# Kernel tuning notes

Hardware: AMD Instinct MI355X
Metric: run time of the kernel (lower is better)

The kernel has to match this reference:

```python
import jax, jax.numpy as jnp
import numpy as np

N, D_IN, D_C, D_Q, K = 4096, 64, 32, 128, 3


def setup_inputs() -> dict:
    key = jax.random.key(0)
    ks = jax.random.split(key, 16)
    rn = lambda k, shp, s: jax.random.normal(k, shp, dtype=jnp.float32) * s
    inp = {
        "x": rn(ks[0], (N, D_IN), 1.0),
        "comms": rn(ks[1], (N, D_C), 0.1),
        # dense positive transition matrix (all entries nonzero -> the
        # trans==0 -> -inf masking step is a faithful no-op here)
        "trans": jax.random.uniform(ks[2], (N, N), dtype=jnp.float32, minval=0.01, maxval=1.0),
        "mask": jnp.ones((N,), dtype=jnp.int32),
        # encoding: Linear(num_inputs + comm_channels, ch_q)
        "W_enc": rn(ks[3], (D_IN + D_C, D_Q), 1.0 / np.sqrt(D_IN + D_C)),
        "b_enc": rn(ks[4], (D_Q,), 0.01),
        # att_decoding[k]: Linear(ch_q, ch_q)
        "W_ad": rn(ks[5], (K, D_Q, D_Q), 1.0 / np.sqrt(D_Q)),
        "b_ad": rn(ks[6], (K, D_Q), 0.01),
        # att[k]: Linear(2*ch_q, 1)
        "w_att": rn(ks[7], (K, 2 * D_Q), 1.0 / np.sqrt(2 * D_Q)),
        "b_att": rn(ks[8], (K,), 0.01),
        # att_vectors[k]: Linear(ch_q, ch_q)
        "W_av": rn(ks[9], (K, D_Q, D_Q), 1.0 / np.sqrt(D_Q)),
        "b_av": rn(ks[10], (K, D_Q), 0.01),
        # decoding: Linear(ch_q, 1)
        "W_dec": rn(ks[11], (D_Q,), 1.0 / np.sqrt(D_Q)),
        "b_dec": rn(ks[12], (), 0.01),
    }
    return inp


def reference(x, comms, trans, mask, W_enc, b_enc, W_ad, b_ad, w_att, b_att,
              W_av, b_av, W_dec, b_dec):
    dq = W_ad.shape[-1]
    # encoding of [node features, communication vector]
    h = jnp.concatenate([x, comms], axis=-1) @ W_enc + b_enc          # (n, dq)
    # trans.transpose(0,1); zeros -> -inf (additive log-mask)
    tb = trans.T
    tb = jnp.where(tb == 0, -jnp.inf, tb)                              # (n, n)
    for k in range(K):
        att = h @ W_ad[k] + b_ad[k]                                    # (n, dq)
        # concat-GAT score: score[i,j] = w_a . att[j] + w_b . att[i] + b
        # (decomposition of Linear(cat(att_t, att_t^T)) -> avoids n x n x 2dq)
        wa, wb = w_att[k, :dq], w_att[k, dq:]
        score = (att @ wb)[:, None] + (att @ wa)[None, :] + b_att[k]   # (n, n)
        focus = jax.nn.softmax(score + tb, axis=1)                     # (n, n)
        v = h @ W_av[k] + b_av[k]                                      # (n, dq)
        h = focus @ v                                                  # (n, dq)
    out = h @ W_dec + b_dec                                            # (n,)
    # final masking (args.rl = False branch): masked nodes -> -inf
    s = out + jnp.where(mask == 0, -jnp.inf, 0.0).astype(out.dtype)
    return s
```

## Files before the change

kernel.cpp:

```cpp
#include <hip/hip_runtime.h>
#include <math.h>

#define N 4096
#define DQ 128
#define DIN 64
#define DC 32
#define NT 9
#define PST9 144
#define PST1 16
#define NIT 256
#define KB 4
#define SW 8
#define ELS 260

typedef __attribute__((ext_vector_type(8))) short short8;
typedef __attribute__((ext_vector_type(8))) _Float16 half8;
typedef __attribute__((ext_vector_type(4))) float f32x4;

__device__ __forceinline__ unsigned short f2h(float x) {
  return __builtin_bit_cast(unsigned short, (_Float16)x);
}
__device__ __forceinline__ void async16(unsigned short* lds, const unsigned short* g) {
  __builtin_amdgcn_global_load_lds(
      (const __attribute__((address_space(1))) void*)g,
      (__attribute__((address_space(3))) void*)lds, 16, 0, 0);
}

__global__ __launch_bounds__(256) void kExp(const float* __restrict__ trans,
                                            unsigned short* __restrict__ Ef) {
  __shared__ float sh[32 * ELS];
  const int tid = threadIdx.x;
  const int ip = blockIdx.x;
  const int kt = blockIdx.y;
  float4 v[8];
#pragma unroll
  for (int p = 0; p < 8; ++p) {
    const int f = p * 256 + tid;
    const int r = f >> 6, c = (f & 63) << 2;
    v[p] = *(const float4*)&trans[((size_t)kt * 32 + r) * N + ip * 256 + c];
  }
#pragma unroll
  for (int p = 0; p < 8; ++p) {
    const int f = p * 256 + tid;
    const int r = f >> 6, c = (f & 63) << 2;
    float4 e;
    e.x = __expf(v[p].x); e.y = __expf(v[p].y);
    e.z = __expf(v[p].z); e.w = __expf(v[p].w);
    *(float4*)&sh[r * ELS + c] = e;
  }
  __syncthreads();
  const int w = tid >> 6, lane = tid & 63;
  const int quad = lane >> 4, l15 = lane & 15;
#pragma unroll
  for (int s = 0; s < 4; ++s) {
    const int col = 64 * w + s * 16 + l15;
    unsigned short hb[8];
#pragma unroll
    for (int jj = 0; jj < 8; ++jj)
      hb[jj] = f2h(sh[(quad * 8 + jj) * ELS + col]);
    const short8 sv = {(short)hb[0], (short)hb[1], (short)hb[2], (short)hb[3],
                       (short)hb[4], (short)hb[5], (short)hb[6], (short)hb[7]};
    const int it = ip * 16 + 4 * w + s;
    *(short8*)(Ef + (((size_t)kt * NIT + it) * 64 + lane) * 8) = sv;
  }
}

__device__ __forceinline__ void v_phase(const float* hs_row, float p,
    const float* __restrict__ W_av_k, const float* __restrict__ b_av_k,
    int r, int d4, unsigned short* shh) {
  float a[4] = {b_av_k[d4], b_av_k[d4 + 1], b_av_k[d4 + 2], b_av_k[d4 + 3]};
  for (int c = 0; c < DQ; ++c) {
    const float hv = hs_row[c];
    const float4 w = *(const float4*)&W_av_k[c * DQ + d4];
    a[0] += hv * w.x; a[1] += hv * w.y; a[2] += hv * w.z; a[3] += hv * w.w;
  }
  const int nt = d4 >> 4;
#pragma unroll
  for (int e = 0; e < 4; ++e)
    shh[nt * 128 + ((d4 + e) & 15) * 8 + r] = f2h(p * a[e]);
  const int c32 = d4 >> 2;
  if (c32 < 16)
    shh[8 * 128 + c32 * 8 + r] = (c32 == 0) ? f2h(p) : 0;
}

__device__ __forceinline__ void v_store(int tid, int blk,
    const unsigned short* shh, unsigned short* __restrict__ Vf) {
  const int kt = blk >> 2, quad = blk & 3;
  if (tid < NT * 16) {
    const int nt = tid >> 4, l15 = tid & 15;
    const size_t dst = (((size_t)kt * NT + nt) * 64 + quad * 16 + l15) * 8;
    *(short8*)(Vf + dst) = *(const short8*)&shh[nt * 128 + l15 * 8];
  }
}

__global__ __launch_bounds__(256) void kVS0(const float* __restrict__ x,
    const float* __restrict__ comms, const float* __restrict__ W_enc,
    const float* __restrict__ b_enc, const float* __restrict__ W_ad_k,
    const float* __restrict__ wa, const float* __restrict__ W_av_k,
    const float* __restrict__ b_av_k, unsigned short* __restrict__ Vf) {
  __shared__ float xs[8][96];
  __shared__ float hs[8][DQ];
  __shared__ float u[DQ];
  __shared__ float pb[8];
  __shared__ __align__(16) unsigned short shh[NT * 128];
  const int tid = threadIdx.x;
  const int blk = blockIdx.x;
  if (tid < 128) {
    const float4 v = *(const float4*)&x[(size_t)blk * 8 * DIN + tid * 4];
    const int idx = tid * 4, r = idx >> 6, c = idx & 63;
    xs[r][c] = v.x; xs[r][c + 1] = v.y; xs[r][c + 2] = v.z; xs[r][c + 3] = v.w;
  } else if (tid < 192) {
    const int t = tid - 128;
    const float4 v = *(const float4*)&comms[(size_t)blk * 8 * DC + t * 4];
    const int idx = t * 4, r = idx >> 5, c = idx & 31;
    xs[r][64 + c] = v.x; xs[r][64 + c + 1] = v.y; xs[r][64 + c + 2] = v.z; xs[r][64 + c + 3] = v.w;
  }
  if (tid < DQ) {
    float s = 0.f;
    const float* wrow = &W_ad_k[tid * DQ];
    for (int q = 0; q < DQ; ++q) s += wrow[q] * wa[q];
    u[tid] = s;
  }
  __syncthreads();
  const int r = tid >> 5;
  const int c32 = tid & 31;
  const int d4 = c32 * 4;
  {
    float a0 = b_enc[d4], a1 = b_enc[d4 + 1], a2 = b_enc[d4 + 2], a3 = b_enc[d4 + 3];
    for (int c = 0; c < 96; ++c) {
      const float hv = xs[r][c];
      const float4 w = *(const float4*)&W_enc[c * DQ + d4];
      a0 += hv * w.x; a1 += hv * w.y; a2 += hv * w.z; a3 += hv * w.w;
    }
    hs[r][d4] = a0; hs[r][d4 + 1] = a1; hs[r][d4 + 2] = a2; hs[r][d4 + 3] = a3;
  }
  __syncthreads();
  float part = 0.f;
  for (int c = c32; c < DQ; c += 32) part += hs[r][c] * u[c];
#pragma unroll
  for (int m = 16; m > 0; m >>= 1) part += __shfl_xor(part, m, 32);
  if (c32 == 0) pb[r] = __expf(part);
  __syncthreads();
  v_phase(hs[r], pb[r], W_av_k, b_av_k, r, d4, shh);
  __syncthreads();
  v_store(tid, blk, shh, Vf);
}

__global__ __launch_bounds__(256) void kVSR(const float* __restrict__ P,
    const float* __restrict__ W_ad_k, const float* __restrict__ wa,
    const float* __restrict__ W_av_k, const float* __restrict__ b_av_k,
    unsigned short* __restrict__ Vf) {
  __shared__ float hs[8][DQ];
  __shared__ float u[DQ];
  __shared__ float pb[8];
  __shared__ __align__(16) unsigned short shh[NT * 128];
  const int tid = threadIdx.x;
  const int r = tid >> 5;
  const int c32 = tid & 31;
  const int d4 = c32 * 4;
  const int j = blockIdx.x * 8 + r;
  if (tid < DQ) {
    float s = 0.f;
    const float* wrow = &W_ad_k[tid * DQ];
    for (int q = 0; q < DQ; ++q) s += wrow[q] * wa[q];
    u[tid] = s;
  }
  float4 num = {0.f, 0.f, 0.f, 0.f};
  float den = 0.f;
#pragma unroll
  for (int s = 0; s < KB; ++s) {
    const float* b = &P[((size_t)s * N + j) * PST9];
    const float4 v = *(const float4*)&b[d4];
    num.x += v.x; num.y += v.y; num.z += v.z; num.w += v.w;
    den += b[128];
  }
  const float inv = 1.f / den;
  hs[r][d4] = num.x * inv; hs[r][d4 + 1] = num.y * inv;
  hs[r][d4 + 2] = num.z * inv; hs[r][d4 + 3] = num.w * inv;
  __syncthreads();
  float part = 0.f;
  for (int c = c32; c < DQ; c += 32) part += hs[r][c] * u[c];
#pragma unroll
  for (int m = 16; m > 0; m >>= 1) part += __shfl_xor(part, m, 32);
  if (c32 == 0) pb[r] = __expf(part);
  __syncthreads();
  v_phase(hs[r], pb[r], W_av_k, b_av_k, r, d4, shh);
  __syncthreads();
  v_store(tid, blockIdx.x, shh, Vf);
}

__global__ __launch_bounds__(256) void kVSRc(const float* __restrict__ P,
    const float* __restrict__ W_ad_k, const float* __restrict__ wa,
    const float* __restrict__ W_av_k, const float* __restrict__ b_av_k,
    const float* __restrict__ W_dec, unsigned short* __restrict__ Vc) {
  __shared__ float hs[8][DQ];
  __shared__ float u[DQ];
  __shared__ float pb[8];
  const int tid = threadIdx.x;
  const int r = tid >> 5;
  const int c32 = tid & 31;
  const int d4 = c32 * 4;
  const int j = blockIdx.x * 8 + r;
  if (tid < DQ) {
    float s = 0.f;
    const float* wrow = &W_ad_k[tid * DQ];
    for (int q = 0; q < DQ; ++q) s += wrow[q] * wa[q];
    u[tid] = s;
  }
  float4 num = {0.f, 0.f, 0.f, 0.f};
  float den = 0.f;
#pragma unroll
  for (int s = 0; s < KB; ++s) {
    const float* b = &P[((size_t)s * N + j) * PST9];
    const float4 v = *(const float4*)&b[d4];
    num.x += v.x; num.y += v.y; num.z += v.z; num.w += v.w;
    den += b[128];
  }
  const float inv = 1.f / den;
  hs[r][d4] = num.x * inv; hs[r][d4 + 1] = num.y * inv;
  hs[r][d4 + 2] = num.z * inv; hs[r][d4 + 3] = num.w * inv;
  __syncthreads();
  float part = 0.f;
  for (int c = c32; c < DQ; c += 32) part += hs[r][c] * u[c];
#pragma unroll
  for (int m = 16; m > 0; m >>= 1) part += __shfl_xor(part, m, 32);
  if (c32 == 0) pb[r] = __expf(part);
  __syncthreads();
  float a[4] = {b_av_k[d4], b_av_k[d4 + 1], b_av_k[d4 + 2], b_av_k[d4 + 3]};
  for (int c = 0; c < DQ; ++c) {
    const float hv = hs[r][c];
    const float4 w = *(const float4*)&W_av_k[c * DQ + d4];
    a[0] += hv * w.x; a[1] += hv * w.y; a[2] += hv * w.z; a[3] += hv * w.w;
  }
  float vd = a[0] * W_dec[d4] + a[1] * W_dec[d4 + 1]
           + a[2] * W_dec[d4 + 2] + a[3] * W_dec[d4 + 3];
#pragma unroll
  for (int m = 16; m > 0; m >>= 1) vd += __shfl_xor(vd, m, 32);
  const float p = pb[r];
  if (c32 < 16) {
    const int blk = blockIdx.x;
    const size_t ix = (((size_t)(blk >> 2)) * 64 + (blk & 3) * 16 + c32) * 8 + r;
    Vc[ix] = (c32 == 0) ? f2h(p * vd) : (c32 == 1) ? f2h(p) : 0;
  }
}

template <int NTT, int PST>
__global__ __launch_bounds__(256) void kGemmR(
    const unsigned short* __restrict__ Ef, const unsigned short* __restrict__ Vf,
    float* __restrict__ P) {
  __shared__ __align__(16) unsigned short lds[4 * 2 * NTT * 512];
  const int tid = threadIdx.x;
  const int w = tid >> 6, lane = tid & 63;
  const int quad = lane >> 4, l15 = lane & 15;
  const int it0 = blockIdx.x * 2;
  const size_t ktw = (size_t)blockIdx.y * (4 * SW) + w * SW;
  unsigned short* myL = lds + w * (2 * NTT * 512);

  f32x4 acc[2][NTT];
#pragma unroll
  for (int ti = 0; ti < 2; ++ti)
#pragma unroll
    for (int nt = 0; nt < NTT; ++nt) acc[ti][nt] = (f32x4){0.f, 0.f, 0.f, 0.f};

#pragma unroll
  for (int c = 0; c < NTT; ++c)
    async16(myL + c * 512, Vf + (ktw * NTT + c) * 512 + lane * 8);
  half8 A0[2], A1[2];
#pragma unroll
  for (int ti = 0; ti < 2; ++ti)
    A0[ti] = __builtin_bit_cast(half8,
        *(const short8*)(Ef + ((ktw * NIT + it0 + ti) * 64 + lane) * 8));

#pragma unroll
  for (int t = 0; t < SW; ++t) {
    if (t + 1 < SW) {
      const size_t ktn = ktw + t + 1;
#pragma unroll
      for (int c = 0; c < NTT; ++c)
        async16(myL + ((t + 1) & 1) * NTT * 512 + c * 512,
                Vf + (ktn * NTT + c) * 512 + lane * 8);
#pragma unroll
      for (int ti = 0; ti < 2; ++ti)
        A1[ti] = __builtin_bit_cast(half8,
            *(const short8*)(Ef + ((ktn * NIT + it0 + ti) * 64 + lane) * 8));
      __builtin_amdgcn_s_waitcnt(0xF70 | (NTT + 2));
    } else {
      __builtin_amdgcn_s_waitcnt(0xF70);
    }
    const unsigned short* bb = myL + (t & 1) * NTT * 512;
#pragma unroll
    for (int nt = 0; nt < NTT; ++nt) {
      const half8 Bh = __builtin_bit_cast(half8,
          *(const short8*)(bb + nt * 512 + lane * 8));
      acc[0][nt] = __builtin_amdgcn_mfma_f32_16x16x32_f16(A0[0], Bh, acc[0][nt], 0, 0, 0);
      acc[1][nt] = __builtin_amdgcn_mfma_f32_16x16x32_f16(A0[1], Bh, acc[1][nt], 0, 0, 0);
    }
    if (t + 1 < SW) { A0[0] = A1[0]; A0[1] = A1[1]; }
  }
  __syncthreads();
  float* lf = (float*)lds;
#pragma unroll
  for (int ti = 0; ti < 2; ++ti)
#pragma unroll
    for (int nt = 0; nt < NTT; ++nt) {
      float4 v; v.x = acc[ti][nt][0]; v.y = acc[ti][nt][1];
      v.z = acc[ti][nt][2]; v.w = acc[ti][nt][3];
      *(float4*)&lf[(w * 2 * NTT + ti * NTT + nt) * 256 + lane * 4] = v;
    }
  __syncthreads();
  float* Pb = P + (size_t)blockIdx.y * N * PST;
  for (int p = w; p < 2 * NTT; p += 4) {
    const int ti = p / NTT, nt = p % NTT;
    float4 s = {0.f, 0.f, 0.f, 0.f};
#pragma unroll
    for (int wv = 0; wv < 4; ++wv) {
      const float4 v = *(const float4*)&lf[(wv * 2 * NTT + p) * 256 + lane * 4];
      s.x += v.x; s.y += v.y; s.z += v.z; s.w += v.w;
    }
    const float sr[4] = {s.x, s.y, s.z, s.w};
    if (NTT == 1 || nt != 8 || l15 == 0) {
#pragma unroll
      for (int r = 0; r < 4; ++r) {
        const int i = (it0 + ti) * 16 + quad * 4 + r;
        Pb[(size_t)i * PST + nt * 16 + l15] = sr[r];
      }
    }
  }
}

__global__ __launch_bounds__(256) void kOut(const float* __restrict__ P3,
    const float* __restrict__ b_dec, const int* __restrict__ mask,
    float* __restrict__ out) {
  const int i = blockIdx.x * 256 + threadIdx.x;
  float num = 0.f, den = 0.f;
#pragma unroll
  for (int s = 0; s < KB; ++s) {
    const float* b = &P3[((size_t)s * N + i) * PST1];
    num += b[0];
    den += b[1];
  }
  out[i] = (mask[i] == 0) ? -INFINITY : num / den + b_dec[0];
}

extern "C" void kernel_launch(void* const* d_in, const int* in_sizes, int n_in,
                              void* d_out, int out_size, void* d_ws, size_t ws_size,
                              hipStream_t stream) {
  (void)in_sizes; (void)n_in; (void)out_size; (void)ws_size;
  const float* x     = (const float*)d_in[0];
  const float* comms = (const float*)d_in[1];
  const float* trans = (const float*)d_in[2];
  const int*   mask  = (const int*)d_in[3];
  const float* W_enc = (const float*)d_in[4];
  const float* b_enc = (const float*)d_in[5];
  const float* W_ad  = (const float*)d_in[6];
  const float* w_att = (const float*)d_in[8];
  const float* W_av  = (const float*)d_in[10];
  const float* b_av  = (const float*)d_in[11];
  const float* W_dec = (const float*)d_in[12];
  const float* b_dec = (const float*)d_in[13];
  float* out         = (float*)d_out;

  char* ws = (char*)d_ws;
  unsigned short* Vf = (unsigned short*)ws;  ws += (size_t)(N / 32) * NT * 512 * 2;
  unsigned short* Vc = (unsigned short*)ws;  ws += (size_t)(N / 32) * 512 * 2;
  unsigned short* Ef = (unsigned short*)ws;  ws += (size_t)N * N * 2;
  float* P  = (float*)ws;                    ws += (size_t)KB * N * PST9 * 4;
  float* P3 = (float*)ws;

  kExp<<<dim3(16, 128), 256, 0, stream>>>(trans, Ef);
  kVS0<<<N / 8, 256, 0, stream>>>(x, comms, W_enc, b_enc, W_ad, w_att,
                                  W_av, b_av, Vf);
  kGemmR<NT, PST9><<<dim3(NIT / 2, KB), 256, 0, stream>>>(Ef, Vf, P);

  kVSR<<<N / 8, 256, 0, stream>>>(P, W_ad + (size_t)1 * DQ * DQ,
                                  w_att + 2 * DQ, W_av + (size_t)1 * DQ * DQ,
                                  b_av + DQ, Vf);
  kGemmR<NT, PST9><<<dim3(NIT / 2, KB), 256, 0, stream>>>(Ef, Vf, P);

  kVSRc<<<N / 8, 256, 0, stream>>>(P, W_ad + (size_t)2 * DQ * DQ,
                                   w_att + 4 * DQ, W_av + (size_t)2 * DQ * DQ,
                                   b_av + 2 * DQ, W_dec, Vc);
  kGemmR<1, PST1><<<dim3(NIT / 2, KB), 256, 0, stream>>>(Ef, Vc, P3);

  kOut<<<N / 256, 256, 0, stream>>>(P3, b_dec, mask, out);
}
```

Before: 215.4 us.

## Fuse exp and first-layer prep kernels, drop LDS staging, fuse final GEMM with output

Merges the trans-exp conversion and the first V-projection kernel into one launch that branches on block index. The kGemmR B fragments now load straight from global memory into registers, with register double-buffering in place of async LDS staging, and an occupancy hint is added. The last narrow GEMM and the kOut reduction become a single kGemmO kernel that reduces across waves in LDS and writes the masked ratio directly. This removes two launches and the P3 round trip through memory, at the cost of more register pressure and no LDS reuse for B.

```diff
diff --git a/kernel.cpp b/kernel.cpp
--- a/kernel.cpp
+++ b/kernel.cpp
@@ -7,7 +7,6 @@
 #define DC 32
 #define NT 9
 #define PST9 144
-#define PST1 16
 #define NIT 256
 #define KB 4
 #define SW 8
@@ -20,49 +19,8 @@
 __device__ __forceinline__ unsigned short f2h(float x) {
   return __builtin_bit_cast(unsigned short, (_Float16)x);
 }
-__device__ __forceinline__ void async16(unsigned short* lds, const unsigned short* g) {
-  __builtin_amdgcn_global_load_lds(
-      (const __attribute__((address_space(1))) void*)g,
-      (__attribute__((address_space(3))) void*)lds, 16, 0, 0);
-}
-
-__global__ __launch_bounds__(256) void kExp(const float* __restrict__ trans,
-                                            unsigned short* __restrict__ Ef) {
-  __shared__ float sh[32 * ELS];
-  const int tid = threadIdx.x;
-  const int ip = blockIdx.x;
-  const int kt = blockIdx.y;
-  float4 v[8];
-#pragma unroll
-  for (int p = 0; p < 8; ++p) {
-    const int f = p * 256 + tid;
-    const int r = f >> 6, c = (f & 63) << 2;
-    v[p] = *(const float4*)&trans[((size_t)kt * 32 + r) * N + ip * 256 + c];
-  }
-#pragma unroll
-  for (int p = 0; p < 8; ++p) {
-    const int f = p * 256 + tid;
-    const int r = f >> 6, c = (f & 63) << 2;
-    float4 e;
-    e.x = __expf(v[p].x); e.y = __expf(v[p].y);
-    e.z = __expf(v[p].z); e.w = __expf(v[p].w);
-    *(float4*)&sh[r * ELS + c] = e;
-  }
-  __syncthreads();
-  const int w = tid >> 6, lane = tid & 63;
-  const int quad = lane >> 4, l15 = lane & 15;
-#pragma unroll
-  for (int s = 0; s < 4; ++s) {
-    const int col = 64 * w + s * 16 + l15;
-    unsigned short hb[8];
-#pragma unroll
-    for (int jj = 0; jj < 8; ++jj)
-      hb[jj] = f2h(sh[(quad * 8 + jj) * ELS + col]);
-    const short8 sv = {(short)hb[0], (short)hb[1], (short)hb[2], (short)hb[3],
-                       (short)hb[4], (short)hb[5], (short)hb[6], (short)hb[7]};
-    const int it = ip * 16 + 4 * w + s;
-    *(short8*)(Ef + (((size_t)kt * NIT + it) * 64 + lane) * 8) = sv;
-  }
+__device__ __forceinline__ half8 ldfrag(const unsigned short* p) {
+  return __builtin_bit_cast(half8, *(const short8*)p);
 }
 
 __device__ __forceinline__ void v_phase(const float* hs_row, float p,
@@ -93,57 +51,98 @@
   }
 }
 
-__global__ __launch_bounds__(256) void kVS0(const float* __restrict__ x,
-    const float* __restrict__ comms, const float* __restrict__ W_enc,
-    const float* __restrict__ b_enc, const float* __restrict__ W_ad_k,
-    const float* __restrict__ wa, const float* __restrict__ W_av_k,
-    const float* __restrict__ b_av_k, unsigned short* __restrict__ Vf) {
-  __shared__ float xs[8][96];
-  __shared__ float hs[8][DQ];
-  __shared__ float u[DQ];
-  __shared__ float pb[8];
-  __shared__ __align__(16) unsigned short shh[NT * 128];
+__global__ __launch_bounds__(256) void kPre(
+    const float* __restrict__ trans, unsigned short* __restrict__ Ef,
+    const float* __restrict__ x, const float* __restrict__ comms,
+    const float* __restrict__ W_enc, const float* __restrict__ b_enc,
+    const float* __restrict__ W_ad_k, const float* __restrict__ wa,
+    const float* __restrict__ W_av_k, const float* __restrict__ b_av_k,
+    unsigned short* __restrict__ Vf) {
+  __shared__ __align__(16) char smem[32 * ELS * 4];
   const int tid = threadIdx.x;
-  const int blk = blockIdx.x;
-  if (tid < 128) {
-    const float4 v = *(const float4*)&x[(size_t)blk * 8 * DIN + tid * 4];
-    const int idx = tid * 4, r = idx >> 6, c = idx & 63;
-    xs[r][c] = v.x; xs[r][c + 1] = v.y; xs[r][c + 2] = v.z; xs[r][c + 3] = v.w;
-  } else if (tid < 192) {
-    const int t = tid - 128;
-    const float4 v = *(const float4*)&comms[(size_t)blk * 8 * DC + t * 4];
-    const int idx = t * 4, r = idx >> 5, c = idx & 31;
-    xs[r][64 + c] = v.x; xs[r][64 + c + 1] = v.y; xs[r][64 + c + 2] = v.z; xs[r][64 + c + 3] = v.w;
-  }
-  if (tid < DQ) {
-    float s = 0.f;
-    const float* wrow = &W_ad_k[tid * DQ];
-    for (int q = 0; q < DQ; ++q) s += wrow[q] * wa[q];
-    u[tid] = s;
-  }
-  __syncthreads();
-  const int r = tid >> 5;
-  const int c32 = tid & 31;
-  const int d4 = c32 * 4;
-  {
-    float a0 = b_enc[d4], a1 = b_enc[d4 + 1], a2 = b_enc[d4 + 2], a3 = b_enc[d4 + 3];
-    for (int c = 0; c < 96; ++c) {
-      const float hv = xs[r][c];
-      const float4 w = *(const float4*)&W_enc[c * DQ + d4];
-      a0 += hv * w.x; a1 += hv * w.y; a2 += hv * w.z; a3 += hv * w.w;
-    }
-    hs[r][d4] = a0; hs[r][d4 + 1] = a1; hs[r][d4 + 2] = a2; hs[r][d4 + 3] = a3;
-  }
-  __syncthreads();
-  float part = 0.f;
-  for (int c = c32; c < DQ; c += 32) part += hs[r][c] * u[c];
-#pragma unroll
-  for (int m = 16; m > 0; m >>= 1) part += __shfl_xor(part, m, 32);
-  if (c32 == 0) pb[r] = __expf(part);
-  __syncthreads();
-  v_phase(hs[r], pb[r], W_av_k, b_av_k, r, d4, shh);
-  __syncthreads();
-  v_store(tid, blk, shh, Vf);
+  if (blockIdx.x < 2048) {
+    float* sh = (float*)smem;
+    const int ip = blockIdx.x & 15;
+    const int kt = blockIdx.x >> 4;
+    float4 v[8];
+#pragma unroll
+    for (int p = 0; p < 8; ++p) {
+      const int f = p * 256 + tid;
+      const int r = f >> 6, c = (f & 63) << 2;
+      v[p] = *(const float4*)&trans[((size_t)kt * 32 + r) * N + ip * 256 + c];
+    }
+#pragma unroll
+    for (int p = 0; p < 8; ++p) {
+      const int f = p * 256 + tid;
+      const int r = f >> 6, c = (f & 63) << 2;
+      float4 e;
+      e.x = __expf(v[p].x); e.y = __expf(v[p].y);
+      e.z = __expf(v[p].z); e.w = __expf(v[p].w);
+      *(float4*)&sh[r * ELS + c] = e;
+    }
+    __syncthreads();
+    const int w = tid >> 6, lane = tid & 63;
+    const int quad = lane >> 4, l15 = lane & 15;
+#pragma unroll
+    for (int s = 0; s < 4; ++s) {
+      const int col = 64 * w + s * 16 + l15;
+      unsigned short hb[8];
+#pragma unroll
+      for (int jj = 0; jj < 8; ++jj)
+        hb[jj] = f2h(sh[(quad * 8 + jj) * ELS + col]);
+      const short8 sv = {(short)hb[0], (short)hb[1], (short)hb[2], (short)hb[3],
+                         (short)hb[4], (short)hb[5], (short)hb[6], (short)hb[7]};
+      const int itt = ip * 16 + 4 * w + s;
+      *(short8*)(Ef + (((size_t)kt * NIT + itt) * 64 + lane) * 8) = sv;
+    }
+  } else {
+    const int blk = blockIdx.x - 2048;
+    float(*xs)[96] = (float(*)[96])smem;
+    float(*hs)[DQ] = (float(*)[DQ])(smem + 3072);
+    float* u = (float*)(smem + 7168);
+    float* pb = (float*)(smem + 7680);
+    unsigned short* shh = (unsigned short*)(smem + 7712);
+    if (tid < 128) {
+      const float4 vv = *(const float4*)&x[(size_t)blk * 8 * DIN + tid * 4];
+      const int idx = tid * 4, r = idx >> 6, c = idx & 63;
+      xs[r][c] = vv.x; xs[r][c + 1] = vv.y; xs[r][c + 2] = vv.z; xs[r][c + 3] = vv.w;
+    } else if (tid < 192) {
+      const int t = tid - 128;
+      const float4 vv = *(const float4*)&comms[(size_t)blk * 8 * DC + t * 4];
+      const int idx = t * 4, r = idx >> 5, c = idx & 31;
+      xs[r][64 + c] = vv.x; xs[r][64 + c + 1] = vv.y;
+      xs[r][64 + c + 2] = vv.z; xs[r][64 + c + 3] = vv.w;
+    }
+    if (tid < DQ) {
+      float s = 0.f;
+      const float* wrow = &W_ad_k[tid * DQ];
+      for (int q = 0; q < DQ; ++q) s += wrow[q] * wa[q];
+      u[tid] = s;
+    }
+    __syncthreads();
+    const int r = tid >> 5;
+    const int c32 = tid & 31;
+    const int d4 = c32 * 4;
+    {
+      float a0 = b_enc[d4], a1 = b_enc[d4 + 1], a2 = b_enc[d4 + 2], a3 = b_enc[d4 + 3];
+      for (int c = 0; c < 96; ++c) {
+        const float hv = xs[r][c];
+        const float4 w = *(const float4*)&W_enc[c * DQ + d4];
+        a0 += hv * w.x; a1 += hv * w.y; a2 += hv * w.z; a3 += hv * w.w;
+      }
+      hs[r][d4] = a0; hs[r][d4 + 1] = a1; hs[r][d4 + 2] = a2; hs[r][d4 + 3] = a3;
+    }
+    __syncthreads();
+    float part = 0.f;
+    for (int c = c32; c < DQ; c += 32) part += hs[r][c] * u[c];
+#pragma unroll
+    for (int m = 16; m > 0; m >>= 1) part += __shfl_xor(part, m, 32);
+    if (c32 == 0) pb[r] = __expf(part);
+    __syncthreads();
+    v_phase(hs[r], pb[r], W_av_k, b_av_k, r, d4, shh);
+    __syncthreads();
+    v_store(tid, blk, shh, Vf);
+  }
 }
 
 __global__ __launch_bounds__(256) void kVSR(const float* __restrict__ P,
@@ -245,16 +244,15 @@
 }
 
 template <int NTT, int PST>
-__global__ __launch_bounds__(256) void kGemmR(
+__global__ __launch_bounds__(256, 2) void kGemmR(
     const unsigned short* __restrict__ Ef, const unsigned short* __restrict__ Vf,
     float* __restrict__ P) {
-  __shared__ __align__(16) unsigned short lds[4 * 2 * NTT * 512];
+  __shared__ __align__(16) float lf[4 * 2 * NTT * 256];
   const int tid = threadIdx.x;
   const int w = tid >> 6, lane = tid & 63;
   const int quad = lane >> 4, l15 = lane & 15;
   const int it0 = blockIdx.x * 2;
   const size_t ktw = (size_t)blockIdx.y * (4 * SW) + w * SW;
-  unsigned short* myL = lds + w * (2 * NTT * 512);
 
   f32x4 acc[2][NTT];
 #pragma unroll
@@ -262,43 +260,37 @@
 #pragma unroll
     for (int nt = 0; nt < NTT; ++nt) acc[ti][nt] = (f32x4){0.f, 0.f, 0.f, 0.f};
 
-#pragma unroll
-  for (int c = 0; c < NTT; ++c)
-    async16(myL + c * 512, Vf + (ktw * NTT + c) * 512 + lane * 8);
-  half8 A0[2], A1[2];
-#pragma unroll
-  for (int ti = 0; ti < 2; ++ti)
-    A0[ti] = __builtin_bit_cast(half8,
-        *(const short8*)(Ef + ((ktw * NIT + it0 + ti) * 64 + lane) * 8));
+  const unsigned short* Ap = Ef + (ktw * NIT + it0) * 512 + lane * 8;
+  const unsigned short* Bp = Vf + ktw * (NTT * 512) + lane * 8;
+
+  half8 A0[2], A1[2], B0[NTT], B1[NTT];
+#pragma unroll
+  for (int ti = 0; ti < 2; ++ti) A0[ti] = ldfrag(Ap + ti * 512);
+#pragma unroll
+  for (int nt = 0; nt < NTT; ++nt) B0[nt] = ldfrag(Bp + nt * 512);
 
 #pragma unroll
   for (int t = 0; t < SW; ++t) {
     if (t + 1 < SW) {
-      const size_t ktn = ktw + t + 1;
-#pragma unroll
-      for (int c = 0; c < NTT; ++c)
-        async16(myL + ((t + 1) & 1) * NTT * 512 + c * 512,
-                Vf + (ktn * NTT + c) * 512 + lane * 8);
-#pragma unroll
-      for (int ti = 0; ti < 2; ++ti)
-        A1[ti] = __builtin_bit_cast(half8,
-            *(const short8*)(Ef + ((ktn * NIT + it0 + ti) * 64 + lane) * 8));
-      __builtin_amdgcn_s_waitcnt(0xF70 | (NTT + 2));
-    } else {
-      __builtin_amdgcn_s_waitcnt(0xF70);
-    }
-    const unsigned short* bb = myL + (t & 1) * NTT * 512;
+      const unsigned short* An = Ap + (size_t)(t + 1) * (NIT * 512);
+      const unsigned short* Bn = Bp + (size_t)(t + 1) * (NTT * 512);
+#pragma unroll
+      for (int nt = 0; nt < NTT; ++nt) B1[nt] = ldfrag(Bn + nt * 512);
+#pragma unroll
+      for (int ti = 0; ti < 2; ++ti) A1[ti] = ldfrag(An + ti * 512);
+    }
 #pragma unroll
     for (int nt = 0; nt < NTT; ++nt) {
-      const half8 Bh = __builtin_bit_cast(half8,
-          *(const short8*)(bb + nt * 512 + lane * 8));
-      acc[0][nt] = __builtin_amdgcn_mfma_f32_16x16x32_f16(A0[0], Bh, acc[0][nt], 0, 0, 0);
-      acc[1][nt] = __builtin_amdgcn_mfma_f32_16x16x32_f16(A0[1], Bh, acc[1][nt], 0, 0, 0);
-    }
-    if (t + 1 < SW) { A0[0] = A1[0]; A0[1] = A1[1]; }
-  }
-  __syncthreads();
-  float* lf = (float*)lds;
+      acc[0][nt] = __builtin_amdgcn_mfma_f32_16x16x32_f16(A0[0], B0[nt], acc[0][nt], 0, 0, 0);
+      acc[1][nt] = __builtin_amdgcn_mfma_f32_16x16x32_f16(A0[1], B0[nt], acc[1][nt], 0, 0, 0);
+    }
+    if (t + 1 < SW) {
+      A0[0] = A1[0]; A0[1] = A1[1];
+#pragma unroll
+      for (int nt = 0; nt < NTT; ++nt) B0[nt] = B1[nt];
+    }
+  }
+
 #pragma unroll
   for (int ti = 0; ti < 2; ++ti)
 #pragma unroll
@@ -328,18 +320,44 @@
   }
 }
 
-__global__ __launch_bounds__(256) void kOut(const float* __restrict__ P3,
+__global__ __launch_bounds__(512, 2) void kGemmO(
+    const unsigned short* __restrict__ Ef, const unsigned short* __restrict__ Vc,
     const float* __restrict__ b_dec, const int* __restrict__ mask,
     float* __restrict__ out) {
-  const int i = blockIdx.x * 256 + threadIdx.x;
-  float num = 0.f, den = 0.f;
-#pragma unroll
-  for (int s = 0; s < KB; ++s) {
-    const float* b = &P3[((size_t)s * N + i) * PST1];
-    num += b[0];
-    den += b[1];
-  }
-  out[i] = (mask[i] == 0) ? -INFINITY : num / den + b_dec[0];
+  __shared__ float red[8 * 256];
+  __shared__ float nums[16], dens[16];
+  const int tid = threadIdx.x;
+  const int w = tid >> 6, lane = tid & 63;
+  const int it = blockIdx.x;
+  const int kt0 = w * 16;
+  half8 Af[16], Bf[16];
+#pragma unroll
+  for (int t = 0; t < 16; ++t) {
+    const size_t kt = kt0 + t;
+    Af[t] = ldfrag(Ef + (kt * NIT + it) * 512 + lane * 8);
+    Bf[t] = ldfrag(Vc + kt * 512 + lane * 8);
+  }
+  f32x4 acc = (f32x4){0.f, 0.f, 0.f, 0.f};
+#pragma unroll
+  for (int t = 0; t < 16; ++t)
+    acc = __builtin_amdgcn_mfma_f32_16x16x32_f16(Af[t], Bf[t], acc, 0, 0, 0);
+  float4 v; v.x = acc[0]; v.y = acc[1]; v.z = acc[2]; v.w = acc[3];
+  *(float4*)&red[w * 256 + lane * 4] = v;
+  __syncthreads();
+  if (tid < 256) {
+    const int l = tid & 63, e = tid >> 6;
+    float s = 0.f;
+#pragma unroll
+    for (int ww = 0; ww < 8; ++ww) s += red[ww * 256 + l * 4 + e];
+    const int col = l & 15, row = (l >> 4) * 4 + e;
+    if (col == 0) nums[row] = s;
+    else if (col == 1) dens[row] = s;
+  }
+  __syncthreads();
+  if (tid < 16) {
+    const int i = it * 16 + tid;
+    out[i] = (mask[i] == 0) ? -INFINITY : nums[tid] / dens[tid] + b_dec[0];
+  }
 }
 
 extern "C" void kernel_launch(void* const* d_in, const int* in_sizes, int n_in,
@@ -364,12 +382,10 @@
   unsigned short* Vf = (unsigned short*)ws;  ws += (size_t)(N / 32) * NT * 512 * 2;
   unsigned short* Vc = (unsigned short*)ws;  ws += (size_t)(N / 32) * 512 * 2;
   unsigned short* Ef = (unsigned short*)ws;  ws += (size_t)N * N * 2;
-  float* P  = (float*)ws;                    ws += (size_t)KB * N * PST9 * 4;
-  float* P3 = (float*)ws;
-
-  kExp<<<dim3(16, 128), 256, 0, stream>>>(trans, Ef);
-  kVS0<<<N / 8, 256, 0, stream>>>(x, comms, W_enc, b_enc, W_ad, w_att,
-                                  W_av, b_av, Vf);
+  float* P  = (float*)ws;
+
+  kPre<<<2560, 256, 0, stream>>>(trans, Ef, x, comms, W_enc, b_enc, W_ad,
+                                 w_att, W_av, b_av, Vf);
   kGemmR<NT, PST9><<<dim3(NIT / 2, KB), 256, 0, stream>>>(Ef, Vf, P);
 
   kVSR<<<N / 8, 256, 0, stream>>>(P, W_ad + (size_t)1 * DQ * DQ,
@@ -380,7 +396,5 @@
   kVSRc<<<N / 8, 256, 0, stream>>>(P, W_ad + (size_t)2 * DQ * DQ,
                                    w_att + 4 * DQ, W_av + (size_t)2 * DQ * DQ,
                                    b_av + 2 * DQ, W_dec, Vc);
-  kGemmR<1, PST1><<<dim3(NIT / 2, KB), 256, 0, stream>>>(Ef, Vc, P3);
-
-  kOut<<<N / 256, 256, 0, stream>>>(P3, b_dec, mask, out);
-}
+  kGemmO<<<NIT, 512, 0, stream>>>(Ef, Vc, b_dec, mask, out);
+}
```

Result: slower. 220.0 us (+2.1%).
